# Kernel optimization log

Measured on AMD Instinct MI355X. Metric: run time of the kernel, lower is better.

Reference implementation:

```python
import jax, jax.numpy as jnp
import numpy as np
from jax import lax

B, N, NB = 1, 1600, 200
NOTE, ENC, ENCVEC = 128, 64, 16
OUT, MARGIN, TREG = 11, 32, 32
E = 12
FIN = NOTE + ENC + 2 * TREG + OUT + MARGIN   # 299 = net_params.final.input
SEC = OUT + MARGIN                           # 43 = GatedGraph secondary size
FBH = NOTE + ENC                             # final_beat_hidden_idx
SEQ_IT, G_IT = 2, 3
HEADS_M = 8


def setup_inputs():
    key = jax.random.key(0)
    ks = iter(jax.random.split(key, 64))
    nrm = lambda shape, s=0.05: jax.random.normal(next(ks), shape, jnp.float32) * s
    zeros = lambda shape: jnp.zeros(shape, jnp.float32)
    inp = {}
    inp["note_out"] = jax.random.normal(next(ks), (B, N, NOTE), jnp.float32)
    inp["perf_vec"] = jax.random.normal(next(ks), (B, ENCVEC), jnp.float32)
    inp["res_info"] = jax.random.normal(next(ks), (B, NB, 8), jnp.float32)
    # sparse musical-graph adjacency, one matrix per edge type
    inp["edges"] = (jax.random.uniform(next(ks), (E, N, N)) < 0.004).astype(jnp.float32)
    # sorted beat index per note, every beat non-empty (8 notes per beat)
    inp["beat_numbers"] = jnp.arange(N, dtype=jnp.int32) // (N // NB)
    inp["w_style"] = nrm((ENCVEC, ENC)); inp["b_style"] = zeros((ENC,))
    inp["w_init1"] = nrm((NOTE, ENC)); inp["b_init1"] = zeros((ENC,))
    inp["w_init2"] = nrm((ENC, OUT)); inp["b_init2"] = zeros((OUT,))
    inp["gg_wa"] = nrm((E, FIN, FIN)); inp["gg_ba"] = zeros((FIN,))
    inp["gg_wz"] = nrm((FIN, SEC)); inp["gg_wr"] = nrm((FIN, SEC)); inp["gg_wh"] = nrm((FIN, SEC))
    inp["gg_uz"] = nrm((SEC, SEC)); inp["gg_ur"] = nrm((SEC, SEC)); inp["gg_uh"] = nrm((SEC, SEC))
    inp["att_beat_w"] = nrm((OUT, OUT)); inp["att_beat_b"] = zeros((OUT,)); inp["att_beat_c"] = nrm((1, OUT), 1.0)
    inp["att_marg_w"] = nrm((MARGIN, MARGIN)); inp["att_marg_b"] = zeros((MARGIN,))
    inp["att_marg_c"] = nrm((HEADS_M, MARGIN // HEADS_M), 1.0)
    rnn_in = MARGIN + OUT + 8
    for l, din in ((0, rnn_in), (1, 2 * TREG)):
        for d in "fb":
            inp[f"lstm_wih_{l}{d}"] = nrm((4 * TREG, din))
            inp[f"lstm_whh_{l}{d}"] = nrm((4 * TREG, TREG))
            inp[f"lstm_b_{l}{d}"] = zeros((4 * TREG,))
    inp["w_tempo"] = nrm((2 * TREG, 1)); inp["b_tempo"] = zeros((1,))
    inp["w_fc1"] = nrm((FIN, MARGIN)); inp["b_fc1"] = zeros((MARGIN,))
    inp["w_fc2"] = nrm((MARGIN, OUT - 1)); inp["b_fc2"] = zeros((OUT - 1,))
    return inp


def _gated_graph(h, edges, wa, ba, wz, wr, wh, uz, ur, uh, iters):
    # h: (B,N,FIN), edges: (E,N,N). GGNN update on last SEC features.
    for _ in range(iters):
        agg = jnp.einsum('eij,bid->ebjd', edges, h)          # incoming msgs per edge type
        act = jnp.einsum('ebjd,eds->bjs', agg, wa) + ba      # (B,N,FIN)
        hs = h[..., -SEC:]
        z = jax.nn.sigmoid(act @ wz + hs @ uz)
        r = jax.nn.sigmoid(act @ wr + hs @ ur)
        cand = jnp.tanh(act @ wh + (r * hs) @ uh)
        hs = (1.0 - z) * hs + z * cand
        h = jnp.concatenate([h[..., :-SEC], hs], -1)
    return h


def _seg_attention(x, W, b, ctx, seg, num_seg):
    # ContextAttention pooled per beat segment (make_higher_node).
    Bb, T, D = x.shape
    H, hd = ctx.shape
    a = jnp.tanh(x @ W + b).reshape(Bb, T, H, hd)
    sim = jnp.einsum('bthd,hd->bth', a, ctx)
    def smax(s):  # segment softmax over notes within each beat, (T,H)
        m = jax.ops.segment_max(s, seg, num_segments=num_seg)
        e = jnp.exp(s - m[seg])
        zz = jax.ops.segment_sum(e, seg, num_segments=num_seg)
        return e / zz[seg]
    w = jax.vmap(smax)(sim)                                   # (B,T,H)
    xh = x.reshape(Bb, T, H, hd)
    pool = jax.vmap(lambda wi, xi: jax.ops.segment_sum(wi[:, :, None] * xi, seg, num_segments=num_seg))(w, xh)
    return pool.reshape(Bb, num_seg, D)


def _lstm_dir(x, wih, whh, b, reverse):
    Bb = x.shape[0]; H = whh.shape[1]
    def step(carry, xt):
        h, c = carry
        g = xt @ wih.T + h @ whh.T + b
        i, f, gg, o = jnp.split(g, 4, -1)
        c = jax.nn.sigmoid(f) * c + jax.nn.sigmoid(i) * jnp.tanh(gg)
        h = jax.nn.sigmoid(o) * jnp.tanh(c)
        return (h, c), h
    init = (jnp.zeros((Bb, H), x.dtype), jnp.zeros((Bb, H), x.dtype))
    _, hs = lax.scan(step, init, jnp.swapaxes(x, 0, 1), reverse=reverse)
    return jnp.swapaxes(hs, 0, 1)


def _bilstm(x, layers):
    for (wf, uf, bf, wb, ub, bb) in layers:
        x = jnp.concatenate([_lstm_dir(x, wf, uf, bf, False), _lstm_dir(x, wb, ub, bb, True)], -1)
    return x


def _forward(note_out, perf_vec, res_info, edges, beat_numbers,
             w_style, b_style, w_init1, b_init1, w_init2, b_init2,
             gg_wa, gg_ba, gg_wz, gg_wr, gg_wh, gg_uz, gg_ur, gg_uh,
             att_beat_w, att_beat_b, att_beat_c, att_marg_w, att_marg_b, att_marg_c,
             lstm_wih_0f, lstm_whh_0f, lstm_b_0f, lstm_wih_0b, lstm_whh_0b, lstm_b_0b,
             lstm_wih_1f, lstm_whh_1f, lstm_b_1f, lstm_wih_1b, lstm_whh_1b, lstm_b_1b,
             w_tempo, b_tempo, w_fc1, b_fc1, w_fc2, b_fc2):
    Bb, Nn, _ = note_out.shape
    # style_vector_expandor (dropout = identity in eval), broadcast to notes
    perf_z = jax.nn.relu(perf_vec @ w_style + b_style)
    perf_z = jnp.broadcast_to(perf_z[:, None, :], (Bb, Nn, ENC))
    init_out = jax.nn.relu(note_out @ w_init1 + b_init1) @ w_init2 + b_init2
    beat_hid0 = jnp.zeros((Bb, Nn, 2 * TREG), note_out.dtype)
    margin0 = jnp.zeros((Bb, Nn, MARGIN), note_out.dtype)
    out = jnp.concatenate([note_out, perf_z, beat_hid0, init_out, margin0], -1)  # (B,N,FIN)
    lstm_layers = [(lstm_wih_0f, lstm_whh_0f, lstm_b_0f, lstm_wih_0b, lstm_whh_0b, lstm_b_0b),
                   (lstm_wih_1f, lstm_whh_1f, lstm_b_1f, lstm_wih_1b, lstm_whh_1b, lstm_b_1b)]
    total = [init_out]
    final_out = init_out
    for _ in range(SEQ_IT):
        out = _gated_graph(out, edges, gg_wa, gg_ba, gg_wz, gg_wr, gg_wh, gg_uz, gg_ur, gg_uh, G_IT)
        init_o = out[..., -SEC:-MARGIN]          # (B,N,OUT)
        marg = out[..., -MARGIN:]                # (B,N,MARGIN)
        marg_beat = _seg_attention(marg, att_marg_w, att_marg_b, att_marg_c, beat_numbers, NB)
        out_beat = _seg_attention(init_o, att_beat_w, att_beat_b, att_beat_c, beat_numbers, NB)
        beat_cat = jnp.concatenate([out_beat, marg_beat, res_info], -1)  # (B,NB,51)
        rnn = _bilstm(beat_cat, lstm_layers)                             # (B,NB,64)
        tempo = rnn @ w_tempo + b_tempo                                  # (B,NB,1)
        tempos_sp = tempo[:, beat_numbers, :]    # span_beat_to_note_num
        rnn_sp = rnn[:, beat_numbers, :]
        out = jnp.concatenate([out[..., :FBH], rnn_sp, out[..., -SEC:]], -1)
        other = jax.nn.relu(out @ w_fc1 + b_fc1) @ w_fc2 + b_fc2         # (B,N,OUT-1)
        final_out = jnp.concatenate([tempos_sp, other], -1)              # (B,N,OUT)
        out = jnp.concatenate([out[..., :-SEC], final_out, out[..., -MARGIN:]], -1)
        total.append(final_out)
    return final_out, jnp.stack(total, 0)


def reference(note_out, perf_vec, res_info, edges, beat_numbers,
              w_style, b_style, w_init1, b_init1, w_init2, b_init2,
              gg_wa, gg_ba, gg_wz, gg_wr, gg_wh, gg_uz, gg_ur, gg_uh,
              att_beat_w, att_beat_b, att_beat_c, att_marg_w, att_marg_b, att_marg_c,
              lstm_wih_0f, lstm_whh_0f, lstm_b_0f, lstm_wih_0b, lstm_whh_0b, lstm_b_0b,
              lstm_wih_1f, lstm_whh_1f, lstm_b_1f, lstm_wih_1b, lstm_whh_1b, lstm_b_1b,
              w_tempo, b_tempo, w_fc1, b_fc1, w_fc2, b_fc2):
    return _forward(note_out, perf_vec, res_info, edges, beat_numbers,
                    w_style, b_style, w_init1, b_init1, w_init2, b_init2,
                    gg_wa, gg_ba, gg_wz, gg_wr, gg_wh, gg_uz, gg_ur, gg_uh,
                    att_beat_w, att_beat_b, att_beat_c, att_marg_w, att_marg_b, att_marg_c,
                    lstm_wih_0f, lstm_whh_0f, lstm_b_0f, lstm_wih_0b, lstm_whh_0b, lstm_b_0b,
                    lstm_wih_1f, lstm_whh_1f, lstm_b_1f, lstm_wih_1b, lstm_whh_1b, lstm_b_1b,
                    w_tempo, b_tempo, w_fc1, b_fc1, w_fc2, b_fc2)
```

## Files before the change

### kernel.cpp

```cpp
#include <hip/hip_runtime.h>
#include <stdint.h>

#define NN     1600
#define NBEAT  200
#define FINW   299
#define HSTR   300
#define SECW   43
#define EDG    12
#define C3     129
#define CM     128
#define DEG_CAP 256

#define NB_WA3   450
#define NB_INIT8 200
#define NB_SCAN  2560

#define K1C (-1.4426950408889634f)
#define K2C (-2.8853900817779268f)

#if __has_builtin(__builtin_amdgcn_exp2f)
__device__ __forceinline__ float fexp2(float x){ return __builtin_amdgcn_exp2f(x); }
#else
__device__ __forceinline__ float fexp2(float x){ return exp2f(x); }
#endif
#if __has_builtin(__builtin_amdgcn_rcpf)
__device__ __forceinline__ float frcp(float x){ return __builtin_amdgcn_rcpf(x); }
#else
__device__ __forceinline__ float frcp(float x){ return 1.0f/x; }
#endif

__device__ __forceinline__ float sigm(float x){ return frcp(1.f + fexp2(K1C*x)); }
__device__ __forceinline__ float tanh_(float x){ return __builtin_fmaf(frcp(1.f + fexp2(K2C*x)), 2.f, -1.f); }

__device__ __forceinline__ float gate_scale(int col){
  return (col >= 64 && col < 96) ? K2C : K1C;
}

constexpr size_t OFF_H    = 0;
constexpr size_t OFF_WA3  = OFF_H    + (size_t)NN*HSTR;
constexpr size_t OFF_WA3X = OFF_WA3  + (size_t)EDG*FINW*CM;
constexpr size_t OFF_B3   = OFF_WA3X + (size_t)EDG*FINW;
constexpr size_t OFF_MST  = OFF_B3   + 132;
constexpr size_t OFF_MSTX = OFF_MST  + (size_t)EDG*NN*CM;
constexpr size_t OFF_M3   = OFF_MSTX + (size_t)EDG*NN;
constexpr size_t OFF_M3X  = OFF_M3   + (size_t)EDG*NN*CM;
constexpr size_t OFF_CUR  = OFF_M3X  + (size_t)EDG*NN;
constexpr size_t OFF_ADJR = OFF_CUR  + NN;
constexpr size_t OFF_XW   = OFF_ADJR + (size_t)NN*DEG_CAP;
constexpr size_t OFF_RNN0 = OFF_XW   + (size_t)2*NBEAT*128;
constexpr size_t OFF_RNN1 = OFF_RNN0 + (size_t)NBEAT*64;

__global__ __launch_bounds__(192) void k_setup(
    const float* wa, const float* ba, const float* wz, const float* wr, const float* wh,
    const float* note, const float* pv, const float* w_style, const float* b_style,
    const float* w1, const float* b1, const float* w2, const float* b2,
    const float* edges, float* ws, float* dout){
  int blk = blockIdx.x;
  int t = threadIdx.x;
  __shared__ __align__(16) float smem[2392];
  if (blk < NB_WA3){
    float* lrow = smem;
    int base = blk*8;
    for (int x=t; x<8*299; x+=192){
      int r = x & 7, s = x >> 3;
      int R = base + r;
      float v = 0.f;
      if (R < 3588)       v = wa[(size_t)R*FINW + s];
      else if (R == 3588) v = ba[s];
      lrow[s*8 + r] = v;
    }
    __syncthreads();
    if (t < C3){
      const float* Wp; int cc;
      if (t<43){Wp=wz; cc=t;} else if (t<86){Wp=wr; cc=t-43;} else {Wp=wh; cc=t-86;}
      float acc[8];
      #pragma unroll
      for (int r=0;r<8;r++) acc[r]=0.f;
      for (int s=0;s<FINW;s++){
        float w = Wp[s*43+cc];
        float4 lo = *(const float4*)&lrow[s*8];
        float4 hi = *(const float4*)&lrow[s*8+4];
        acc[0]+=lo.x*w; acc[1]+=lo.y*w; acc[2]+=lo.z*w; acc[3]+=lo.w*w;
        acc[4]+=hi.x*w; acc[5]+=hi.y*w; acc[6]+=hi.z*w; acc[7]+=hi.w*w;
      }
      #pragma unroll
      for (int r=0;r<8;r++){
        int R = base + r;
        if (R < 3588){
          if (t<CM) ws[OFF_WA3 + (size_t)R*CM + t] = acc[r];
          else      ws[OFF_WA3X + R]               = acc[r];
        } else if (R == 3588){
          ws[OFF_B3 + t] = acc[r];
        }
      }
    }
  } else if (blk < NB_WA3 + NB_INIT8){
    float* ln    = smem;
    float* lh1   = smem + 1024;
    float* lo    = smem + 1536;
    float* lperf = smem + 1624;
    int i0 = (blk - NB_WA3)*8;
    for (int x=t; x<8*128; x+=192){
      int r = x >> 7, k = x & 127;
      ln[k*8 + r] = note[(size_t)(i0+r)*128 + k];
    }
    if (t>=64 && t<128){
      int u=t-64;
      float acc=b_style[u];
      for (int k=0;k<16;k++) acc += pv[k]*w_style[k*64+u];
      lperf[u]=fmaxf(acc,0.f);
    }
    __syncthreads();
    if (t<64){
      float acc[8];
      #pragma unroll
      for (int r=0;r<8;r++) acc[r]=b1[t];
      for (int k=0;k<128;k++){
        float w = w1[k*64+t];
        float4 a = *(const float4*)&ln[k*8];
        float4 b = *(const float4*)&ln[k*8+4];
        acc[0]+=a.x*w; acc[1]+=a.y*w; acc[2]+=a.z*w; acc[3]+=a.w*w;
        acc[4]+=b.x*w; acc[5]+=b.y*w; acc[6]+=b.z*w; acc[7]+=b.w*w;
      }
      #pragma unroll
      for (int r=0;r<8;r++) lh1[t*8+r]=fmaxf(acc[r],0.f);
    }
    __syncthreads();
    if (t<88){
      int r = t & 7, c = t >> 3;
      float acc=b2[c];
      for (int k=0;k<64;k++) acc += lh1[k*8+r]*w2[k*11+c];
      lo[r*11+c]=acc;
      dout[17600 + (size_t)(i0+r)*11 + c] = acc;
    }
    __syncthreads();
    #pragma unroll
    for (int r=0;r<8;r++){
      for (int c=t;c<FINW;c+=192){
        float v;
        if (c<128)      v=ln[c*8+r];
        else if (c<192) v=lperf[c-128];
        else if (c<256) v=0.f;
        else if (c<267) v=lo[r*11+(c-256)];
        else            v=0.f;
        ws[OFF_H + (size_t)(i0+r)*HSTR + c]=v;
      }
    }
  } else {
    int* cur  = (int*)(ws + OFF_CUR);
    int* adjr = (int*)(ws + OFF_ADJR);
    const uint4* p = (const uint4*)edges;
    const unsigned int nvec = 7680000u;
    const unsigned int stride = (unsigned int)NB_SCAN*192u;
    unsigned int v0 = (unsigned int)(blk - NB_WA3 - NB_INIT8)*192u + t;
    for (unsigned int b0 = v0; b0 < nvec; b0 += 4u*stride){
      unsigned int v1=b0+stride, v2=b0+2u*stride, v3=b0+3u*stride;
      bool g1=v1<nvec, g2=v2<nvec, g3=v3<nvec;
      uint4 w0 = p[b0];
      uint4 w1v = g1 ? p[v1] : make_uint4(0,0,0,0);
      uint4 w2v = g2 ? p[v2] : make_uint4(0,0,0,0);
      uint4 w3v = g3 ? p[v3] : make_uint4(0,0,0,0);
      uint4 wv[4] = {w0,w1v,w2v,w3v};
      unsigned int vv[4] = {b0,v1,v2,v3};
      #pragma unroll
      for (int u=0; u<4; u++){
        uint4 w = wv[u];
        if ((w.x|w.y|w.z|w.w)==0u) continue;
        unsigned int base = vv[u]*4u;
        unsigned int arr[4]={w.x,w.y,w.z,w.w};
        #pragma unroll
        for (int q=0;q<4;q++){
          if (arr[q]){
            unsigned int idx=base+q;
            unsigned int j=idx%1600u;
            int slot=atomicAdd(&cur[j],1);
            if (slot<DEG_CAP) adjr[j*DEG_CAP + slot]=(int)(idx/1600u);
          }
        }
      }
    }
  }
}

__global__ void k_mstat(float* ws){
  int e = blockIdx.y; int i0 = blockIdx.x*8;
  int t = threadIdx.x;
  __shared__ float lh[8][256];
  __shared__ float lh2[8][44];
  const float* h = ws + OFF_H;
  for (int x=t; x<512; x+=64){
    int r = x>>6, dq = x&63;
    ((float4*)&lh[r][0])[dq] = ((const float4*)(h + (size_t)(i0+r)*HSTR))[dq];
  }
  for (int x=t; x<88; x+=64){
    int r = x/11, dq = x-r*11;
    ((float4*)&lh2[r][0])[dq] = ((const float4*)(h + (size_t)(i0+r)*HSTR + 256))[dq];
  }
  __syncthreads();
  const float* wm = ws + OFF_WA3 + (size_t)e*FINW*CM;
  int c0 = 2*t;
  float acc[8][2];
  #pragma unroll
  for (int r=0;r<8;r++){acc[r][0]=0.f;acc[r][1]=0.f;}
  for (int d=0; d<256; d+=4){
    float4 hv[8];
    #pragma unroll
    for (int r=0;r<8;r++) hv[r] = *(const float4*)&lh[r][d];
    #pragma unroll
    for (int dd=0;dd<4;dd++){
      float2 w = *(const float2*)(wm + (size_t)(d+dd)*CM + c0);
      #pragma unroll
      for (int r=0;r<8;r++){
        float hvv = ((const float*)&hv[r])[dd];
        acc[r][0] += hvv*w.x; acc[r][1] += hvv*w.y;
      }
    }
  }
  float* mst = ws + OFF_MST + ((size_t)e*NN + i0)*CM;
  #pragma unroll
  for (int r=0;r<8;r++) *(float2*)(mst + (size_t)r*CM + c0) = make_float2(acc[r][0],acc[r][1]);
  const float* wd = wm + (size_t)256*CM;
  for (int d=0; d<SECW; d++){
    float2 w = *(const float2*)(wd + (size_t)d*CM + c0);
    #pragma unroll
    for (int r=0;r<8;r++){
      float hvv = lh2[r][d];
      acc[r][0] += hvv*w.x; acc[r][1] += hvv*w.y;
    }
  }
  float* m3 = ws + OFF_M3 + ((size_t)e*NN + i0)*CM;
  #pragma unroll
  for (int r=0;r<8;r++) *(float2*)(m3 + (size_t)r*CM + c0) = make_float2(acc[r][0],acc[r][1]);
  if (t<8){
    const float* wx = ws + OFF_WA3X + (size_t)e*FINW;
    float a=0.f;
    for (int d=0; d<256; d++) a += lh[t][d]*wx[d];
    ws[OFF_MSTX + (size_t)e*NN + i0 + t] = a;
    for (int d=0; d<SECW; d++) a += lh2[t][d]*wx[256+d];
    ws[OFF_M3X + (size_t)e*NN + i0 + t] = a;
  }
}

__global__ void k_m3dyn(float* ws){
  int e=blockIdx.y, i0=blockIdx.x*8, t=threadIdx.x;
  __shared__ float lhs[8][44];
  const float* h = ws + OFF_H;
  for (int x=t; x<8*43; x+=64){ int r=x/43, d=x-r*43; lhs[r][d]=h[(size_t)(i0+r)*HSTR+256+d]; }
  __syncthreads();
  const float* wd  = ws + OFF_WA3 + ((size_t)e*FINW+256)*CM;
  const float* mst = ws + OFF_MST + ((size_t)e*NN+i0)*CM;
  int c0=2*t;
  float acc[8][2];
  #pragma unroll
  for (int r=0;r<8;r++){ float2 m=*(const float2*)(mst+(size_t)r*CM+c0); acc[r][0]=m.x; acc[r][1]=m.y; }
  for (int d=0; d<43; d++){
    float2 w=*(const float2*)(wd + (size_t)d*CM + c0);
    #pragma unroll
    for (int r=0;r<8;r++){ float hv=lhs[r][d]; acc[r][0]+=hv*w.x; acc[r][1]+=hv*w.y; }
  }
  float* m3 = ws + OFF_M3 + ((size_t)e*NN+i0)*CM;
  #pragma unroll
  for (int r=0;r<8;r++) *(float2*)(m3+(size_t)r*CM+c0)=make_float2(acc[r][0],acc[r][1]);
  if (t<8){
    float a = ws[OFF_MSTX + (size_t)e*NN+i0+t];
    const float* wx = ws + OFF_WA3X + (size_t)e*FINW + 256;
    for (int d=0;d<43;d++) a += lhs[t][d]*wx[d];
    ws[OFF_M3X + (size_t)e*NN+i0+t]=a;
  }
}

__global__ void k_agg_gru(float* ws, const float* uz, const float* ur, const float* uh){
  int j=blockIdx.x, t=threadIdx.x;
  __shared__ float lpre[C3];
  __shared__ float lhs[SECW];
  __shared__ float lrh[SECW];
  __shared__ int   ladj[DEG_CAP];
  float* h = ws + OFF_H;
  const int* cur =(const int*)(ws+OFF_CUR);
  const int* adjr=(const int*)(ws+OFF_ADJR) + (size_t)j*DEG_CAP;
  int cnt = cur[j]; if (cnt>DEG_CAP) cnt=DEG_CAP;
  for (int k=t;k<cnt;k+=128) ladj[k]=adjr[k];
  if (t<SECW) lhs[t] = h[(size_t)j*HSTR + 256 + t];
  __syncthreads();
  const float* M3=ws+OFF_M3; const float* M3X=ws+OFF_M3X;
  float a0 = ws[OFF_B3 + t];
  float ax = (t==0)? ws[OFF_B3+128] : 0.f;
  float p1=0.f,p2=0.f,p3=0.f,p4=0.f,p5=0.f,p6=0.f,p7=0.f;
  int k=0;
  for (; k+8<=cnt; k+=8){
    int r0=ladj[k],r1=ladj[k+1],r2=ladj[k+2],r3=ladj[k+3];
    int r4=ladj[k+4],r5=ladj[k+5],r6=ladj[k+6],r7=ladj[k+7];
    a0 += M3[(size_t)r0*CM+t];
    p1 += M3[(size_t)r1*CM+t];
    p2 += M3[(size_t)r2*CM+t];
    p3 += M3[(size_t)r3*CM+t];
    p4 += M3[(size_t)r4*CM+t];
    p5 += M3[(size_t)r5*CM+t];
    p6 += M3[(size_t)r6*CM+t];
    p7 += M3[(size_t)r7*CM+t];
    if (t==0) ax += ((M3X[r0]+M3X[r1])+(M3X[r2]+M3X[r3]))
                  + ((M3X[r4]+M3X[r5])+(M3X[r6]+M3X[r7]));
  }
  for (; k<cnt; k++){ int r=ladj[k]; a0+=M3[(size_t)r*CM+t]; if(t==0) ax+=M3X[r]; }
  a0 += ((p1+p2)+(p3+p4)) + ((p5+p6)+p7);
  lpre[t]=a0; if (t==0) lpre[128]=ax;
  __syncthreads();
  float z=0.f;
  if (t<SECW){
    float az=lpre[t], ar=lpre[43+t];
    for (int d=0;d<SECW;d++){ float hv=lhs[d]; az+=hv*uz[d*43+t]; ar+=hv*ur[d*43+t]; }
    z=sigm(az);
    float r=sigm(ar);
    lrh[t]=r*lhs[t];
  }
  __syncthreads();
  if (t<SECW){
    float ah=lpre[86+t];
    for (int d=0;d<SECW;d++) ah += lrh[d]*uh[d*43+t];
    float cand=tanh_(ah);
    h[(size_t)j*HSTR+256+t] = (1.f-z)*lhs[t] + z*cand;
  }
}

__global__ void k_attn_xw(float* ws, const float* mw, const float* mb, const float* mc,
                          const float* bw, const float* bb, const float* bc,
                          const float* res,
                          const float* w0f, const float* bia0f,
                          const float* w0b, const float* bia0b, float* xw){
  int b=blockIdx.x, t=threadIdx.x;
  float* h=ws+OFF_H;
  __shared__ float sm[8][8];
  __shared__ float wgt[8][8];
  __shared__ float sb[8];
  __shared__ float wb_[8];
  __shared__ float lb[52];
  int n=t>>3, hh=t&7;
  if (t<64){
    const float* mrow = h + (size_t)(b*8+n)*HSTR + 267;
    float sim=0.f;
    for (int d=0;d<4;d++){
      int c=hh*4+d;
      float acc=mb[c];
      for (int k=0;k<32;k++) acc += mrow[k]*mw[k*32+c];
      sim += tanh_(acc)*mc[c];
    }
    sm[n][hh]=sim;
  }
  if (t<8){
    const float* irow = h + (size_t)(b*8+t)*HSTR + 256;
    float sim=0.f;
    for (int d=0;d<11;d++){
      float acc=bb[d];
      for (int k=0;k<11;k++) acc += irow[k]*bw[k*11+d];
      sim += tanh_(acc)*bc[d];
    }
    sb[t]=sim;
  }
  __syncthreads();
  if (t<64){
    float m=-1e30f;
    for (int q=0;q<8;q++) m=fmaxf(m, sm[q][hh]);
    float Z=0.f;
    for (int q=0;q<8;q++) Z+=__expf(sm[q][hh]-m);
    wgt[n][hh]=__expf(sm[n][hh]-m)/Z;
  }
  if (t<8){
    float m=-1e30f;
    for (int q=0;q<8;q++) m=fmaxf(m, sb[q]);
    float Z=0.f;
    for (int q=0;q<8;q++) Z+=__expf(sb[q]-m);
    wb_[t]=__expf(sb[t]-m)/Z;
  }
  __syncthreads();
  if (t<32){
    int hh2=t>>2;
    float acc=0.f;
    for (int q=0;q<8;q++) acc += wgt[q][hh2]* h[(size_t)(b*8+q)*HSTR + 267 + t];
    lb[11+t]=acc;
  }
  if (t<11){
    float acc=0.f;
    for (int q=0;q<8;q++) acc += wb_[q]* h[(size_t)(b*8+q)*HSTR + 256 + t];
    lb[t]=acc;
  }
  if (t<8) lb[43+t]=res[b*8+t];
  __syncthreads();
  float acc0=bia0f[t], acc1=bia0b[t];
  for (int k=0;k<51;k++){
    float v=lb[k];
    acc0 += v*w0f[t*51+k];
    acc1 += v*w0b[t*51+k];
  }
  float sc = gate_scale(t);
  xw[((size_t)t)*NBEAT + b]       = acc0*sc;
  xw[((size_t)(128+t))*NBEAT + b] = acc1*sc;
}

__global__ void k_xw(const float* inp, int din, const float* wf, const float* bf_,
                     const float* wb, const float* bb_, float* xw){
  int bid=blockIdx.x; int tt=bid>>1, dir=bid&1;
  const float* w = dir? wb:wf; const float* bia = dir? bb_:bf_;
  __shared__ float rowl[64];
  int t=threadIdx.x;
  if (t<din) rowl[t]=inp[(size_t)tt*din+t];
  __syncthreads();
  float acc=bia[t];
  for (int k=0;k<din;k++) acc += rowl[k]*w[t*din+k];
  xw[((size_t)(dir*128 + t))*NBEAT + tt] = acc*gate_scale(t);
}

template<int DIR>
__device__ __forceinline__ void chunk8(int c, const float4& A0, const float4& A1,
    const float4& B0, const float4& B1,
    float* hu, float& creg, const float4* rA, const float4* rB,
    float cb1, float cb0, int l, float* out){
  float cxA[8] = {A0.x,A0.y,A0.z,A0.w,A1.x,A1.y,A1.z,A1.w};
  float cxB[8] = {B0.x,B0.y,B0.z,B0.w,B1.x,B1.y,B1.z,B1.w};
  float hst[8];
  #pragma unroll
  for (int u=0; u<8; u++){
    const int e = DIR ? (7-u) : u;
    float av[8], bv[8];
    #pragma unroll
    for (int q=0; q<8; q++){
      av[q] = hu[4*q+0]*rA[q].x + hu[4*q+1]*rA[q].y + hu[4*q+2]*rA[q].z + hu[4*q+3]*rA[q].w;
      bv[q] = hu[4*q+0]*rB[q].x + hu[4*q+1]*rB[q].y + hu[4*q+2]*rB[q].z + hu[4*q+3]*rB[q].w;
    }
    float accA = cxA[e] + (((av[0]+av[1])+(av[2]+av[3])) + ((av[4]+av[5])+(av[6]+av[7])));
    float accB = cxB[e] + (((bv[0]+bv[1])+(bv[2]+bv[3])) + ((bv[4]+bv[5])+(bv[6]+bv[7])));
    float pA  = frcp(1.f + fexp2(accA));
    float rBv = frcp(1.f + fexp2(accB));
    float pB  = __builtin_fmaf(rBv, cb1, cb0);
    float prod = pA * pB;
    float prodIn = __shfl(prod, l & 31, 64);
    creg = __builtin_fmaf(pA, creg, prodIn);
    float T = __builtin_fmaf(frcp(1.f + fexp2(creg)), 2.f, -1.f);
    float hnew = pB * T;
    hst[u] = hnew;
    #pragma unroll
    for (int d=0; d<32; d++)
      hu[d] = __uint_as_float(__builtin_amdgcn_readlane(__float_as_uint(hnew), 32+d));
  }
  if (l >= 32){
    int j = l - 32;
    #pragma unroll
    for (int u=0; u<8; u++){
      int s = c*8 + u;
      int tt = DIR ? (199 - s) : s;
      out[(size_t)tt*64 + DIR*32 + j] = hst[u];
    }
  }
}

template<int DIR>
__device__ __forceinline__ void lstm_scan(const float* xwT, const float* whh, float* out){
  const int l = threadIdx.x;
  const float sB = (l < 32) ? K2C : K1C;
  float4 rA[8], rB[8];
  #pragma unroll
  for (int q=0; q<8; q++){
    float4 a = *(const float4*)&whh[l*32 + q*4];
    float4 b = *(const float4*)&whh[(l+64)*32 + q*4];
    rA[q] = make_float4(a.x*K1C, a.y*K1C, a.z*K1C, a.w*K1C);
    rB[q] = make_float4(b.x*sB,  b.y*sB,  b.z*sB,  b.w*sB);
  }
  const float cb1 = (l < 32) ? (2.f*K2C) : 1.f;
  const float cb0 = (l < 32) ? (-K2C)    : 0.f;
  const float* xA = xwT + ((size_t)DIR*128 + l)*NBEAT;
  const float* xB = xwT + ((size_t)DIR*128 + 64 + l)*NBEAT;
  float hu[32];
  #pragma unroll
  for (int d=0; d<32; d++) hu[d] = 0.f;
  float creg = 0.f;
  float4 A0,A1,B0,B1, P0,P1,Q0,Q1;
#define LOADC(cidx, a0,a1,b0,b1) do {               \
    int _b = DIR ? (192 - (cidx)*8) : ((cidx)*8);   \
    a0 = *(const float4*)&xA[_b];                   \
    a1 = *(const float4*)&xA[_b+4];                 \
    b0 = *(const float4*)&xB[_b];                   \
    b1 = *(const float4*)&xB[_b+4];                 \
  } while(0)
  LOADC(0, A0,A1,B0,B1);
  for (int cc=0; cc<12; cc++){
    int c0 = 2*cc;
    LOADC(c0+1, P0,P1,Q0,Q1);
    chunk8<DIR>(c0,   A0,A1,B0,B1, hu, creg, rA, rB, cb1, cb0, l, out);
    LOADC(c0+2, A0,A1,B0,B1);
    chunk8<DIR>(c0+1, P0,P1,Q0,Q1, hu, creg, rA, rB, cb1, cb0, l, out);
  }
  chunk8<DIR>(24, A0,A1,B0,B1, hu, creg, rA, rB, cb1, cb0, l, out);
#undef LOADC
}

__global__ __launch_bounds__(64,1) void k_scan(const float* xwT, const float* whh_f,
                                               const float* whh_b, float* out){
  if (blockIdx.x == 0) lstm_scan<0>(xwT, whh_f, out);
  else                 lstm_scan<1>(xwT, whh_b, out);
}

__global__ void k_fc(float* ws, const int* bn, const float* w1, const float* b1,
                     const float* w2, const float* b2,
                     const float* wt, const float* bt, float* dout, int it){
  int i=blockIdx.x, t=threadIdx.x;
  __shared__ float row[FINW];
  __shared__ float hid[32];
  __shared__ float fo[11];
  float* h=ws+OFF_H;
  int b = bn[i];
  const float* rnn = ws+OFF_RNN1;
  for (int c=t;c<FINW;c+=64){
    float v;
    if (c>=192 && c<256){ v=rnn[(size_t)b*64 + c-192]; h[(size_t)i*HSTR+c]=v; }
    else v=h[(size_t)i*HSTR+c];
    row[c]=v;
  }
  float tv = rnn[(size_t)b*64 + t]*wt[t];
  #pragma unroll
  for (int off=32; off; off>>=1) tv += __shfl_xor(tv, off, 64);
  __syncthreads();
  if (t<32){
    float acc=b1[t];
    for (int k=0;k<FINW;k++) acc += row[k]*w1[k*32+t];
    hid[t]=fmaxf(acc,0.f);
  }
  __syncthreads();
  if (t<10){
    float acc=b2[t];
    for (int m=0;m<32;m++) acc += hid[m]*w2[m*10+t];
    fo[1+t]=acc;
  }
  if (t==0) fo[0]=tv + bt[0];
  __syncthreads();
  if (t<11){
    float v=fo[t];
    h[(size_t)i*HSTR+256+t]=v;
    dout[(size_t)(2+it)*17600 + i*11 + t]=v;
    if (it==1) dout[i*11+t]=v;
  }
}

extern "C" void kernel_launch(void* const* d_in, const int* in_sizes, int n_in,
                              void* d_out, int out_size, void* d_ws, size_t ws_size,
                              hipStream_t stream){
  (void)in_sizes; (void)n_in; (void)out_size; (void)ws_size;
  float* ws=(float*)d_ws;
  const float* note    =(const float*)d_in[0];
  const float* pv      =(const float*)d_in[1];
  const float* res     =(const float*)d_in[2];
  const float* edges   =(const float*)d_in[3];
  const int*   bn      =(const int*)d_in[4];
  const float* w_style =(const float*)d_in[5];
  const float* b_style =(const float*)d_in[6];
  const float* w_init1 =(const float*)d_in[7];
  const float* b_init1 =(const float*)d_in[8];
  const float* w_init2 =(const float*)d_in[9];
  const float* b_init2 =(const float*)d_in[10];
  const float* gg_wa   =(const float*)d_in[11];
  const float* gg_ba   =(const float*)d_in[12];
  const float* gg_wz   =(const float*)d_in[13];
  const float* gg_wr   =(const float*)d_in[14];
  const float* gg_wh   =(const float*)d_in[15];
  const float* gg_uz   =(const float*)d_in[16];
  const float* gg_ur   =(const float*)d_in[17];
  const float* gg_uh   =(const float*)d_in[18];
  const float* abw     =(const float*)d_in[19];
  const float* abb     =(const float*)d_in[20];
  const float* abc     =(const float*)d_in[21];
  const float* amw     =(const float*)d_in[22];
  const float* amb     =(const float*)d_in[23];
  const float* amc     =(const float*)d_in[24];
  const float* wih0f   =(const float*)d_in[25];
  const float* whh0f   =(const float*)d_in[26];
  const float* b0f     =(const float*)d_in[27];
  const float* wih0b   =(const float*)d_in[28];
  const float* whh0b   =(const float*)d_in[29];
  const float* b0b     =(const float*)d_in[30];
  const float* wih1f   =(const float*)d_in[31];
  const float* whh1f   =(const float*)d_in[32];
  const float* b1f     =(const float*)d_in[33];
  const float* wih1b   =(const float*)d_in[34];
  const float* whh1b   =(const float*)d_in[35];
  const float* b1b     =(const float*)d_in[36];
  const float* w_tempo =(const float*)d_in[37];
  const float* b_tempo =(const float*)d_in[38];
  const float* w_fc1   =(const float*)d_in[39];
  const float* b_fc1   =(const float*)d_in[40];
  const float* w_fc2   =(const float*)d_in[41];
  const float* b_fc2   =(const float*)d_in[42];
  float* dout=(float*)d_out;

  hipMemsetAsync(ws+OFF_CUR, 0, NN*sizeof(int), stream);
  k_setup<<<NB_WA3+NB_INIT8+NB_SCAN,192,0,stream>>>(
      gg_wa,gg_ba,gg_wz,gg_wr,gg_wh,
      note,pv,w_style,b_style,w_init1,b_init1,w_init2,b_init2,
      edges,ws,dout);

  for (int it=0; it<2; it++){
    k_mstat<<<dim3(200,12),64,0,stream>>>(ws);
    k_agg_gru<<<NN,128,0,stream>>>(ws,gg_uz,gg_ur,gg_uh);
    for (int g=1; g<3; g++){
      k_m3dyn<<<dim3(200,12),64,0,stream>>>(ws);
      k_agg_gru<<<NN,128,0,stream>>>(ws,gg_uz,gg_ur,gg_uh);
    }
    k_attn_xw<<<NBEAT,128,0,stream>>>(ws,amw,amb,amc,abw,abb,abc,res,
                                      wih0f,b0f,wih0b,b0b,ws+OFF_XW);
    k_scan<<<2,64,0,stream>>>(ws+OFF_XW,whh0f,whh0b,ws+OFF_RNN0);
    k_xw<<<2*NBEAT,128,0,stream>>>(ws+OFF_RNN0,64,wih1f,b1f,wih1b,b1b,ws+OFF_XW);
    k_scan<<<2,64,0,stream>>>(ws+OFF_XW,whh1f,whh1b,ws+OFF_RNN1);
    k_fc<<<NN,64,0,stream>>>(ws,bn,w_fc1,b_fc1,w_fc2,b_fc2,w_tempo,b_tempo,dout,it);
  }
}
```

Measured before the change: 755.8 us.

## Hoist static hidden-state message projection out of iteration loop

Splits the per-edge projection of the hidden state into a part over columns 0-191, computed once after setup because those columns do not change between outer iterations, and a part over columns 192-255 that is recomputed only before the second iteration. The dynamic 43-column part is still handled by k_m3dyn on every graph step. Node tiles grow from 8 to 16 rows per block, halving the block count and reusing each weight load across more rows. It also lowers the setup scan block count. The change relies on columns 0-191 staying constant across iterations and on 64-element columns being updated only between iterations, and the larger tile raises register pressure.

```diff
diff --git a/kernel.cpp b/kernel.cpp
--- a/kernel.cpp
+++ b/kernel.cpp
@@ -13,7 +13,7 @@
 
 #define NB_WA3   450
 #define NB_INIT8 200
-#define NB_SCAN  2560
+#define NB_SCAN  1910
 
 #define K1C (-1.4426950408889634f)
 #define K2C (-2.8853900817779268f)
@@ -182,35 +182,30 @@
   }
 }
 
-__global__ void k_mstat(float* ws){
-  int e = blockIdx.y; int i0 = blockIdx.x*8;
+__global__ void k_mstat_s(float* ws){
+  int e = blockIdx.y; int i0 = blockIdx.x*16;
   int t = threadIdx.x;
-  __shared__ float lh[8][256];
-  __shared__ float lh2[8][44];
+  __shared__ float lh[16][192];
   const float* h = ws + OFF_H;
-  for (int x=t; x<512; x+=64){
-    int r = x>>6, dq = x&63;
+  for (int x=t; x<16*48; x+=64){
+    int r = x/48, dq = x%48;
     ((float4*)&lh[r][0])[dq] = ((const float4*)(h + (size_t)(i0+r)*HSTR))[dq];
-  }
-  for (int x=t; x<88; x+=64){
-    int r = x/11, dq = x-r*11;
-    ((float4*)&lh2[r][0])[dq] = ((const float4*)(h + (size_t)(i0+r)*HSTR + 256))[dq];
   }
   __syncthreads();
   const float* wm = ws + OFF_WA3 + (size_t)e*FINW*CM;
   int c0 = 2*t;
-  float acc[8][2];
-  #pragma unroll
-  for (int r=0;r<8;r++){acc[r][0]=0.f;acc[r][1]=0.f;}
-  for (int d=0; d<256; d+=4){
-    float4 hv[8];
-    #pragma unroll
-    for (int r=0;r<8;r++) hv[r] = *(const float4*)&lh[r][d];
+  float acc[16][2];
+  #pragma unroll
+  for (int r=0;r<16;r++){acc[r][0]=0.f;acc[r][1]=0.f;}
+  for (int d=0; d<192; d+=4){
+    float4 hv[16];
+    #pragma unroll
+    for (int r=0;r<16;r++) hv[r] = *(const float4*)&lh[r][d];
     #pragma unroll
     for (int dd=0;dd<4;dd++){
       float2 w = *(const float2*)(wm + (size_t)(d+dd)*CM + c0);
       #pragma unroll
-      for (int r=0;r<8;r++){
+      for (int r=0;r<16;r++){
         float hvv = ((const float*)&hv[r])[dd];
         acc[r][0] += hvv*w.x; acc[r][1] += hvv*w.y;
       }
@@ -218,50 +213,76 @@
   }
   float* mst = ws + OFF_MST + ((size_t)e*NN + i0)*CM;
   #pragma unroll
-  for (int r=0;r<8;r++) *(float2*)(mst + (size_t)r*CM + c0) = make_float2(acc[r][0],acc[r][1]);
-  const float* wd = wm + (size_t)256*CM;
-  for (int d=0; d<SECW; d++){
-    float2 w = *(const float2*)(wd + (size_t)d*CM + c0);
-    #pragma unroll
-    for (int r=0;r<8;r++){
-      float hvv = lh2[r][d];
-      acc[r][0] += hvv*w.x; acc[r][1] += hvv*w.y;
-    }
-  }
-  float* m3 = ws + OFF_M3 + ((size_t)e*NN + i0)*CM;
-  #pragma unroll
-  for (int r=0;r<8;r++) *(float2*)(m3 + (size_t)r*CM + c0) = make_float2(acc[r][0],acc[r][1]);
-  if (t<8){
+  for (int r=0;r<16;r++) *(float2*)(mst + (size_t)r*CM + c0) = make_float2(acc[r][0],acc[r][1]);
+  if (t<16){
     const float* wx = ws + OFF_WA3X + (size_t)e*FINW;
     float a=0.f;
-    for (int d=0; d<256; d++) a += lh[t][d]*wx[d];
+    for (int d=0; d<192; d++) a += lh[t][d]*wx[d];
     ws[OFF_MSTX + (size_t)e*NN + i0 + t] = a;
-    for (int d=0; d<SECW; d++) a += lh2[t][d]*wx[256+d];
-    ws[OFF_M3X + (size_t)e*NN + i0 + t] = a;
+  }
+}
+
+__global__ void k_mstat64(float* ws){
+  int e = blockIdx.y; int i0 = blockIdx.x*16;
+  int t = threadIdx.x;
+  __shared__ float lh[16][64];
+  const float* h = ws + OFF_H;
+  for (int x=t; x<16*16; x+=64){
+    int r = x>>4, dq = x&15;
+    ((float4*)&lh[r][0])[dq] = ((const float4*)(h + (size_t)(i0+r)*HSTR + 192))[dq];
+  }
+  __syncthreads();
+  const float* wm = ws + OFF_WA3 + ((size_t)e*FINW + 192)*CM;
+  int c0 = 2*t;
+  float* mst = ws + OFF_MST + ((size_t)e*NN + i0)*CM;
+  float acc[16][2];
+  #pragma unroll
+  for (int r=0;r<16;r++){ float2 m=*(const float2*)(mst+(size_t)r*CM+c0); acc[r][0]=m.x; acc[r][1]=m.y; }
+  for (int d=0; d<64; d+=4){
+    float4 hv[16];
+    #pragma unroll
+    for (int r=0;r<16;r++) hv[r] = *(const float4*)&lh[r][d];
+    #pragma unroll
+    for (int dd=0;dd<4;dd++){
+      float2 w = *(const float2*)(wm + (size_t)(d+dd)*CM + c0);
+      #pragma unroll
+      for (int r=0;r<16;r++){
+        float hvv = ((const float*)&hv[r])[dd];
+        acc[r][0] += hvv*w.x; acc[r][1] += hvv*w.y;
+      }
+    }
+  }
+  #pragma unroll
+  for (int r=0;r<16;r++) *(float2*)(mst + (size_t)r*CM + c0) = make_float2(acc[r][0],acc[r][1]);
+  if (t<16){
+    const float* wx = ws + OFF_WA3X + (size_t)e*FINW + 192;
+    float a = ws[OFF_MSTX + (size_t)e*NN + i0 + t];
+    for (int d=0; d<64; d++) a += lh[t][d]*wx[d];
+    ws[OFF_MSTX + (size_t)e*NN + i0 + t] = a;
   }
 }
 
 __global__ void k_m3dyn(float* ws){
-  int e=blockIdx.y, i0=blockIdx.x*8, t=threadIdx.x;
-  __shared__ float lhs[8][44];
+  int e=blockIdx.y, i0=blockIdx.x*16, t=threadIdx.x;
+  __shared__ float lhs[16][44];
   const float* h = ws + OFF_H;
-  for (int x=t; x<8*43; x+=64){ int r=x/43, d=x-r*43; lhs[r][d]=h[(size_t)(i0+r)*HSTR+256+d]; }
+  for (int x=t; x<16*43; x+=64){ int r=x/43, d=x-r*43; lhs[r][d]=h[(size_t)(i0+r)*HSTR+256+d]; }
   __syncthreads();
   const float* wd  = ws + OFF_WA3 + ((size_t)e*FINW+256)*CM;
   const float* mst = ws + OFF_MST + ((size_t)e*NN+i0)*CM;
   int c0=2*t;
-  float acc[8][2];
-  #pragma unroll
-  for (int r=0;r<8;r++){ float2 m=*(const float2*)(mst+(size_t)r*CM+c0); acc[r][0]=m.x; acc[r][1]=m.y; }
+  float acc[16][2];
+  #pragma unroll
+  for (int r=0;r<16;r++){ float2 m=*(const float2*)(mst+(size_t)r*CM+c0); acc[r][0]=m.x; acc[r][1]=m.y; }
   for (int d=0; d<43; d++){
     float2 w=*(const float2*)(wd + (size_t)d*CM + c0);
     #pragma unroll
-    for (int r=0;r<8;r++){ float hv=lhs[r][d]; acc[r][0]+=hv*w.x; acc[r][1]+=hv*w.y; }
+    for (int r=0;r<16;r++){ float hv=lhs[r][d]; acc[r][0]+=hv*w.x; acc[r][1]+=hv*w.y; }
   }
   float* m3 = ws + OFF_M3 + ((size_t)e*NN+i0)*CM;
   #pragma unroll
-  for (int r=0;r<8;r++) *(float2*)(m3+(size_t)r*CM+c0)=make_float2(acc[r][0],acc[r][1]);
-  if (t<8){
+  for (int r=0;r<16;r++) *(float2*)(m3+(size_t)r*CM+c0)=make_float2(acc[r][0],acc[r][1]);
+  if (t<16){
     float a = ws[OFF_MSTX + (size_t)e*NN+i0+t];
     const float* wx = ws + OFF_WA3X + (size_t)e*FINW + 256;
     for (int d=0;d<43;d++) a += lhs[t][d]*wx[d];
@@ -594,12 +615,12 @@
       gg_wa,gg_ba,gg_wz,gg_wr,gg_wh,
       note,pv,w_style,b_style,w_init1,b_init1,w_init2,b_init2,
       edges,ws,dout);
+  k_mstat_s<<<dim3(100,12),64,0,stream>>>(ws);
 
   for (int it=0; it<2; it++){
-    k_mstat<<<dim3(200,12),64,0,stream>>>(ws);
-    k_agg_gru<<<NN,128,0,stream>>>(ws,gg_uz,gg_ur,gg_uh);
-    for (int g=1; g<3; g++){
-      k_m3dyn<<<dim3(200,12),64,0,stream>>>(ws);
+    if (it==1) k_mstat64<<<dim3(100,12),64,0,stream>>>(ws);
+    for (int g=0; g<3; g++){
+      k_m3dyn<<<dim3(100,12),64,0,stream>>>(ws);
       k_agg_gru<<<NN,128,0,stream>>>(ws,gg_uz,gg_ur,gg_uh);
     }
     k_attn_xw<<<NBEAT,128,0,stream>>>(ws,amw,amb,amc,abw,abb,abc,res,
```

New measurement: 804.9 us. +6.5%, slower.
